# Kernel tuning notes

Measured on AMD Instinct MI355X. Metric: run time of the kernel, lower is better.

## Reference

```python
import jax, jax.numpy as jnp
from jax import lax
import numpy as np

B, T, D, U, K = 32, 1000, 512, 5, 3  # batch, frames, idim, upsample_times, conv kernel (l_order+r_order+1)
THRESHOLD = 1.0
TAIL = 0.45


def setup_inputs() -> dict:
    key = jax.random.key(0)
    ks = jax.random.split(key, 6)
    return {
        "encoder_out": jax.random.normal(ks[0], (B, T, D), jnp.float32),
        "mask": jnp.ones((B, 1, T), jnp.float32),
        "conv_w": jax.random.normal(ks[1], (D, D, K), jnp.float32) * 0.02,  # torch Conv1d [out,in,k]
        "conv_b": jnp.zeros((D,), jnp.float32),
        "up_w": jax.random.normal(ks[2], (D, D, U), jnp.float32) * 0.02,    # torch ConvTranspose1d [in,out,k]
        "up_b": jnp.zeros((D,), jnp.float32),
        "w1": jax.random.normal(ks[3], (D,), jnp.float32) * 0.05,           # cif_output Linear(D,1)
        "b1": jnp.zeros((), jnp.float32),
        "w2": jax.random.normal(ks[4], (D,), jnp.float32) * 0.05,           # cif_output2 Linear(D,1)
        "b2": jnp.zeros((), jnp.float32),
    }


def _cif(hidden, alphas, threshold):
    # hidden: [B, Tt, D], alphas: [B, Tt]
    Bb, Tt, Dd = hidden.shape

    def step(carry, inp):
        integrate, frame = carry
        alpha, h_t = inp  # [B], [B, D]
        dist_completion = 1.0 - integrate
        integrate = integrate + alpha
        fires_t = integrate
        fire = integrate >= threshold
        integrate = jnp.where(fire, integrate - 1.0, integrate)
        cur = jnp.where(fire, dist_completion, alpha)
        frame_out = frame + cur[:, None] * h_t
        frame = jnp.where(fire[:, None], (alpha - cur)[:, None] * h_t, frame_out)
        return (integrate, frame), (fires_t, frame_out)

    init = (jnp.zeros((Bb,), hidden.dtype), jnp.zeros((Bb, Dd), hidden.dtype))
    _, (fires, frames) = lax.scan(step, init, (alphas.T, jnp.swapaxes(hidden, 0, 1)))
    fires = fires.T                      # [B, Tt]
    frames = jnp.swapaxes(frames, 0, 1)  # [B, Tt, D]

    fire_mask = fires >= threshold

    def gather_b(frames_b, mask_b):
        pos = jnp.cumsum(mask_b.astype(jnp.int32)) - 1
        pos = jnp.where(mask_b, pos, Tt)  # non-fires -> out of range, dropped
        return jnp.zeros((Tt, Dd), frames_b.dtype).at[pos].set(frames_b, mode='drop')

    acoustic = jax.vmap(gather_b)(frames, fire_mask)  # [B, Tt, D] zero-padded
    return acoustic, fires


def reference(encoder_out, mask, conv_w, conv_b, up_w, up_b, w1, b1, w2, b2):
    Bb, Tt, Dd = encoder_out.shape
    context = jnp.swapaxes(encoder_out, 1, 2)           # [B, D, T]
    queries = jnp.pad(context, ((0, 0), (0, 0), (1, 1)))  # ConstantPad1d((1,1))
    conv = lax.conv_general_dilated(queries, conv_w, (1,), 'VALID',
                                    dimension_numbers=('NCH', 'OIH', 'NCH'))
    output = jax.nn.relu(conv + conv_b[None, :, None])  # [B, D, T]

    # ConvTranspose1d(stride=kernel=U, pad=0): non-overlapping -> einsum
    out2 = jnp.einsum('bit,ioj->btjo', output, up_w).reshape(Bb, Tt * U, Dd) + up_b  # [B, T*U, D]
    alphas2 = jax.nn.relu(jax.nn.sigmoid(out2 @ w2 + b2) * 1.0 - 0.0)  # smooth_factor2=1, noise_threshold2=0
    mask2 = jnp.swapaxes(jnp.broadcast_to(mask, (Bb, U, Tt)), 1, 2).reshape(Bb, Tt * U)
    alphas2 = alphas2 * mask2
    token_num2 = alphas2.sum(-1)

    h1 = jnp.swapaxes(output, 1, 2)  # [B, T, D]
    alphas = jax.nn.relu(jax.nn.sigmoid(h1 @ w1 + b1) * 1.0 - 0.0)  # smooth_factor=1, noise_threshold=0
    maskT = jnp.swapaxes(mask, 1, 2)[..., 0]  # [B, T]
    alphas = alphas * maskT

    # tail_process_fn (tail_threshold=0.45, mask given)
    zeros_t = jnp.zeros((Bb, 1), alphas.dtype)
    ones_t = jnp.ones((Bb, 1), alphas.dtype)
    mask_1 = jnp.concatenate([maskT, zeros_t], axis=1)
    mask_2 = jnp.concatenate([ones_t, maskT], axis=1)
    tail_add = (mask_2 - mask_1) * TAIL
    alphas_t = jnp.concatenate([alphas, zeros_t], axis=1) + tail_add  # [B, T+1]
    hidden = jnp.concatenate([encoder_out, jnp.zeros((Bb, 1, Dd), encoder_out.dtype)], axis=1)
    token_num = jnp.floor(alphas_t.sum(-1))

    acoustic_embeds, cif_peak = _cif(hidden, alphas_t, THRESHOLD)
    return acoustic_embeds, token_num, alphas_t, cif_peak, token_num2
```

## Files before the change

### kernel.cpp

```cpp
#include <hip/hip_runtime.h>
#include <math.h>

#define TB 32
#define TT 1000
#define TD 512
#define TU 5
#define TT1 1001

#define OFF_ACC  0
#define OFF_TOKN 16400384
#define OFF_ALPH 16400416
#define OFF_PEAK 16432448
#define OFF_TOK2 16464480

typedef _Float16 half8 __attribute__((ext_vector_type(8)));
typedef _Float16 half2t __attribute__((ext_vector_type(2)));
typedef float float4t __attribute__((ext_vector_type(4)));

typedef __attribute__((address_space(3))) uint32_t lds_u32_t;
typedef __attribute__((address_space(1))) const uint32_t g_u32_t;
#define GLOAD_LDS(gp, lp) __builtin_amdgcn_global_load_lds((g_u32_t*)(gp), (lds_u32_t*)(lp), 16, 0, 0)

#define BSTR 72
#define ASTR 200
#define EROWS 1032

#define WS_ARAW1 0
#define WS_ARAW2 32000
#define WS_VMAT  192000
#define WS_C2    194560
#define WS_WA    194564
#define WS_WB    226596
#define WS_FIRE  258628
#define WS_NF    290660
#define WS_ENCS_BYTES 1163264ull
#define WS_CWS_BYTES  (WS_ENCS_BYTES + 76059648ull)
#define WS_NEED_BYTES (WS_CWS_BYTES + 3276800ull)

__global__ __launch_bounds__(256) void kzero(float* araw1, float* araw2, float* tok2) {
    int idx = blockIdx.x * 256 + threadIdx.x;
    int stride = gridDim.x * 256;
    for (int i = idx; i < TB * TT; i += stride) araw1[i] = 0.f;
    for (int i = idx; i < TB * TT * TU; i += stride) araw2[i] = 0.f;
    if (idx < TB) tok2[idx] = 0.f;
}

__global__ __launch_bounds__(256) void kc2(const float* __restrict__ up_b, const float* __restrict__ w2,
                                           const float* __restrict__ b2, float* __restrict__ c2out) {
    int tid = threadIdx.x;
    float p = 0.f;
    for (int o = tid; o < TD; o += 256) p += up_b[o] * w2[o];
#pragma unroll
    for (int m = 1; m < 64; m <<= 1) p += __shfl_xor(p, m);
    __shared__ float wsum[4];
    if ((tid & 63) == 0) wsum[tid >> 6] = p;
    __syncthreads();
    if (tid == 0) c2out[0] = b2[0] + wsum[0] + wsum[1] + wsum[2] + wsum[3];
}

__global__ __launch_bounds__(64) void kv(const float* __restrict__ up_w, const float* __restrict__ w2,
                                         float* __restrict__ vmat) {
    int i = blockIdx.x, lane = threadIdx.x;
    float s0 = 0, s1 = 0, s2 = 0, s3 = 0, s4 = 0;
    for (int o = lane; o < TD; o += 64) {
        float w = w2[o];
        const float* p = up_w + (size_t)i * (TD * TU) + o * TU;
        s0 += p[0] * w; s1 += p[1] * w; s2 += p[2] * w; s3 += p[3] * w; s4 += p[4] * w;
    }
#pragma unroll
    for (int m = 1; m < 64; m <<= 1) {
        s0 += __shfl_xor(s0, m); s1 += __shfl_xor(s1, m); s2 += __shfl_xor(s2, m);
        s3 += __shfl_xor(s3, m); s4 += __shfl_xor(s4, m);
    }
    if (lane == 0) {
        float* d = vmat + i * TU;
        d[0] = s0; d[1] = s1; d[2] = s2; d[3] = s3; d[4] = s4;
    }
}

#define FILL_BLOCKS (256 + 1024)
__global__ __launch_bounds__(256) void kfill(float* araw1, float* araw2, float* tok2,
                                             _Float16* encs) {
    int bid = blockIdx.x, tid = threadIdx.x;
    if (bid < 256) {
        int idx = bid * 256 + tid;
        int stride = 256 * 256;
        for (int i = idx; i < TB * TT; i += stride) araw1[i] = 0.f;
        for (int i = idx; i < TB * TT * TU; i += stride) araw2[i] = 0.f;
        if (idx < TB) tok2[idx] = 0.f;
    } else {
        uint32_t* p = (uint32_t*)encs;
        int idx = (bid - 256) * 256 + tid;
        int stride = 1024 * 256;
        const int total = 512 * 32 * 36;
        for (int u = idx; u < total; u += stride) {
            int bic = u / (32 * 36);
            int r = (u / 36) % 32;
            int w = u % 36;
            int row = (r == 0) ? 0 : 1000 + r;
            p[((size_t)bic * EROWS + row) * 36 + w] = 0u;
        }
    }
}

#define WV_BLOCKS (TD + TD)
__global__ __launch_bounds__(64) void kwv(const float* __restrict__ up_w, const float* __restrict__ w2,
                                          const float* __restrict__ cw,
                                          float* __restrict__ vmat, _Float16* __restrict__ cws) {
    int bid = blockIdx.x, lane = threadIdx.x;
    if (bid < TD) {
        int i = bid;
        float s0 = 0, s1 = 0, s2 = 0, s3 = 0, s4 = 0;
        for (int o = lane; o < TD; o += 64) {
            float w = w2[o];
            const float* p = up_w + (size_t)i * (TD * TU) + o * TU;
            s0 += p[0] * w; s1 += p[1] * w; s2 += p[2] * w; s3 += p[3] * w; s4 += p[4] * w;
        }
#pragma unroll
        for (int m = 1; m < 64; m <<= 1) {
            s0 += __shfl_xor(s0, m); s1 += __shfl_xor(s1, m); s2 += __shfl_xor(s2, m);
            s3 += __shfl_xor(s3, m); s4 += __shfl_xor(s4, m);
        }
        if (lane == 0) {
            float* d = vmat + i * TU;
            d[0] = s0; d[1] = s1; d[2] = s2; d[3] = s3; d[4] = s4;
        }
    } else {
        int o = bid - TD;
        for (int u = lane; u < 16 * 32 * 3; u += 64) {
            int tap = u % 3, pos = (u / 3) % 32, ic = u / 96;
            float x = cw[((size_t)o * TD + ic * 32 + pos) * 3 + tap];
            _Float16 h = (_Float16)x;
            _Float16 l = (_Float16)(x - (float)h);
            size_t base = (((size_t)(o >> 5) * 16 + ic) * 32 + (o & 31)) * ASTR + tap * 64;
            cws[base + pos] = h;
            cws[base + 32 + pos] = l;
        }
    }
}

__global__ __launch_bounds__(256) void ksplitE(const float* __restrict__ enc, _Float16* __restrict__ encs) {
    int t = blockIdx.x, b = blockIdx.y, tid = threadIdx.x;
    int c = tid * 2;
    const float2 x2 = *(const float2*)&enc[((size_t)b * TT + t) * TD + c];
    float x0 = x2.x, x1 = x2.y;
    _Float16 h0 = (_Float16)x0, h1 = (_Float16)x1;
    _Float16 l0 = (_Float16)(x0 - (float)h0), l1 = (_Float16)(x1 - (float)h1);
    int ic = c >> 5, pos = c & 31;
    size_t base = ((size_t)(b * 16 + ic) * EROWS + 1 + t) * BSTR + pos;
    half2t hh; hh[0] = h0; hh[1] = h1;
    half2t ll; ll[0] = l0; ll[1] = l1;
    *(half2t*)&encs[base] = hh;
    *(half2t*)&encs[base + 32] = ll;
}

__global__ __launch_bounds__(256, 2) void kconvMD(const _Float16* __restrict__ encs,
                                                  const _Float16* __restrict__ cws,
                                                  const float* __restrict__ cb, const float* __restrict__ w1,
                                                  const float* __restrict__ vmat,
                                                  float* __restrict__ araw1, float* __restrict__ araw2) {
    __shared__ _Float16 sB[258 * BSTR];
    __shared__ _Float16 sA[64 * ASTR];

    const int tid = threadIdx.x;
    const int t0 = blockIdx.x * 256;
    const int oc = blockIdx.y;
    const int b = blockIdx.z;
    const int o0 = oc * 64;
    const int wv = tid >> 6, lane = tid & 63;
    const int q = lane >> 4, l15 = lane & 15;

    float4t acc[4][4];
#pragma unroll
    for (int i = 0; i < 4; ++i)
#pragma unroll
        for (int j = 0; j < 4; ++j) acc[i][j] = (float4t){0.f, 0.f, 0.f, 0.f};

    for (int ic = 0; ic < 16; ++ic) {
        __syncthreads();
        const _Float16* gB = encs + ((size_t)(b * 16 + ic) * EROWS + t0) * BSTR;
        for (int c = tid; c < 2322; c += 256) GLOAD_LDS(gB + c * 8, &sB[c * 8]);
        const _Float16* gA0 = cws + ((size_t)((oc * 2 + 0) * 16 + ic) * 32) * ASTR;
        const _Float16* gA1 = cws + ((size_t)((oc * 2 + 1) * 16 + ic) * 32) * ASTR;
        for (int c = tid; c < 800; c += 256) GLOAD_LDS(gA0 + c * 8, &sA[c * 8]);
        for (int c = tid; c < 800; c += 256) GLOAD_LDS(gA1 + c * 8, &sA[6400 + c * 8]);
        __syncthreads();
#pragma unroll
        for (int tap = 0; tap < 3; ++tap) {
            half8 Bh[4], Bl[4];
#pragma unroll
            for (int tt = 0; tt < 4; ++tt) {
                int s = wv * 64 + tt * 16 + l15 + tap;
                Bh[tt] = *(const half8*)&sB[s * BSTR + q * 8];
                Bl[tt] = *(const half8*)&sB[s * BSTR + 32 + q * 8];
            }
#pragma unroll
            for (int ot = 0; ot < 4; ++ot) {
                const int orow = ot * 16 + l15;
                half8 Ah = *(const half8*)&sA[orow * ASTR + tap * 64 + q * 8];
                half8 Al = *(const half8*)&sA[orow * ASTR + tap * 64 + 32 + q * 8];
#pragma unroll
                for (int tt = 0; tt < 4; ++tt) {
                    acc[ot][tt] = __builtin_amdgcn_mfma_f32_16x16x32_f16(Ah, Bh[tt], acc[ot][tt], 0, 0, 0);
                    acc[ot][tt] = __builtin_amdgcn_mfma_f32_16x16x32_f16(Ah, Bl[tt], acc[ot][tt], 0, 0, 0);
                    acc[ot][tt] = __builtin_amdgcn_mfma_f32_16x16x32_f16(Al, Bh[tt], acc[ot][tt], 0, 0, 0);
                }
            }
        }
    }

#pragma unroll
    for (int tt = 0; tt < 4; ++tt) {
        int t = t0 + wv * 64 + tt * 16 + l15;
        float s1 = 0.f, sa = 0.f, sb = 0.f, sc = 0.f, sd = 0.f, se = 0.f;
#pragma unroll
        for (int ot = 0; ot < 4; ++ot) {
#pragma unroll
            for (int r = 0; r < 4; ++r) {
                int o = o0 + ot * 16 + q * 4 + r;
                float rv = fmaxf(acc[ot][tt][r] + cb[o], 0.f);
                s1 = fmaf(w1[o], rv, s1);
                const float* vp = &vmat[o * 5];
                sa = fmaf(vp[0], rv, sa); sb = fmaf(vp[1], rv, sb);
                sc = fmaf(vp[2], rv, sc); sd = fmaf(vp[3], rv, sd);
                se = fmaf(vp[4], rv, se);
            }
        }
        s1 += __shfl_xor(s1, 16); sa += __shfl_xor(sa, 16); sb += __shfl_xor(sb, 16);
        sc += __shfl_xor(sc, 16); sd += __shfl_xor(sd, 16); se += __shfl_xor(se, 16);
        s1 += __shfl_xor(s1, 32); sa += __shfl_xor(sa, 32); sb += __shfl_xor(sb, 32);
        sc += __shfl_xor(sc, 32); sd += __shfl_xor(sd, 32); se += __shfl_xor(se, 32);
        if (q == 0 && t < TT) {
            atomicAdd(&araw1[b * TT + t], s1);
            float* p2 = &araw2[(b * TT + t) * 5];
            atomicAdd(p2 + 0, sa); atomicAdd(p2 + 1, sb); atomicAdd(p2 + 2, sc);
            atomicAdd(p2 + 3, sd); atomicAdd(p2 + 4, se);
        }
    }
}

__global__ __launch_bounds__(256, 3) void kconvM(const float* __restrict__ enc, const float* __restrict__ cw,
                                                 const float* __restrict__ cb, const float* __restrict__ w1,
                                                 const float* __restrict__ vmat,
                                                 float* __restrict__ araw1, float* __restrict__ araw2) {
    __shared__ _Float16 sB[258 * BSTR];
    __shared__ _Float16 sA[32 * ASTR];

    const int tid = threadIdx.x;
    const int t0 = blockIdx.x * 256;
    const int o0 = blockIdx.y * 32;
    const int b = blockIdx.z;
    const int wv = tid >> 6, lane = tid & 63;
    const int q = lane >> 4, l15 = lane & 15;

    float4t acc[2][4];
#pragma unroll
    for (int i = 0; i < 2; ++i)
#pragma unroll
        for (int j = 0; j < 4; ++j) acc[i][j] = (float4t){0.f, 0.f, 0.f, 0.f};

    for (int i0 = 0; i0 < TD; i0 += 32) {
        __syncthreads();
        for (int u = tid; u < 258 * 16; u += 256) {
            int s = u >> 4, ii2 = (u & 15) << 1;
            int t = t0 - 1 + s;
            float x0 = 0.f, x1 = 0.f;
            if (t >= 0 && t < TT) {
                const float* p = &enc[((size_t)b * TT + t) * TD + i0 + ii2];
                x0 = p[0]; x1 = p[1];
            }
            _Float16 h0 = (_Float16)x0, h1 = (_Float16)x1;
            _Float16 l0 = (_Float16)(x0 - (float)h0), l1 = (_Float16)(x1 - (float)h1);
            half2t hh; hh[0] = h0; hh[1] = h1;
            half2t ll; ll[0] = l0; ll[1] = l1;
            *(half2t*)&sB[s * BSTR + ii2] = hh;
            *(half2t*)&sB[s * BSTR + 32 + ii2] = ll;
        }
        for (int u = tid; u < 32 * 16; u += 256) {
            int o = u >> 4, ii2 = (u & 15) << 1;
            const float* p = &cw[((size_t)(o0 + o) * TD + i0 + ii2) * 3];
#pragma unroll
            for (int k = 0; k < 3; ++k) {
                float x0 = p[k], x1 = p[3 + k];
                _Float16 h0 = (_Float16)x0, h1 = (_Float16)x1;
                _Float16 l0 = (_Float16)(x0 - (float)h0), l1 = (_Float16)(x1 - (float)h1);
                half2t hh; hh[0] = h0; hh[1] = h1;
                half2t ll; ll[0] = l0; ll[1] = l1;
                *(half2t*)&sA[o * ASTR + k * 64 + ii2] = hh;
                *(half2t*)&sA[o * ASTR + k * 64 + 32 + ii2] = ll;
            }
        }
        __syncthreads();
#pragma unroll
        for (int tap = 0; tap < 3; ++tap) {
            half8 Bh[4], Bl[4];
#pragma unroll
            for (int tt = 0; tt < 4; ++tt) {
                int s = wv * 64 + tt * 16 + l15 + tap;
                Bh[tt] = *(const half8*)&sB[s * BSTR + q * 8];
                Bl[tt] = *(const half8*)&sB[s * BSTR + 32 + q * 8];
            }
#pragma unroll
            for (int ot = 0; ot < 2; ++ot) {
                const int orow = ot * 16 + l15;
                half8 Ah = *(const half8*)&sA[orow * ASTR + tap * 64 + q * 8];
                half8 Al = *(const half8*)&sA[orow * ASTR + tap * 64 + 32 + q * 8];
#pragma unroll
                for (int tt = 0; tt < 4; ++tt) {
                    acc[ot][tt] = __builtin_amdgcn_mfma_f32_16x16x32_f16(Ah, Bh[tt], acc[ot][tt], 0, 0, 0);
                    acc[ot][tt] = __builtin_amdgcn_mfma_f32_16x16x32_f16(Ah, Bl[tt], acc[ot][tt], 0, 0, 0);
                    acc[ot][tt] = __builtin_amdgcn_mfma_f32_16x16x32_f16(Al, Bh[tt], acc[ot][tt], 0, 0, 0);
                }
            }
        }
    }

#pragma unroll
    for (int tt = 0; tt < 4; ++tt) {
        int t = t0 + wv * 64 + tt * 16 + l15;
        float s1 = 0.f, sa = 0.f, sb = 0.f, sc = 0.f, sd = 0.f, se = 0.f;
#pragma unroll
        for (int ot = 0; ot < 2; ++ot) {
#pragma unroll
            for (int r = 0; r < 4; ++r) {
                int o = o0 + ot * 16 + q * 4 + r;
                float rv = fmaxf(acc[ot][tt][r] + cb[o], 0.f);
                s1 = fmaf(w1[o], rv, s1);
                const float* vp = &vmat[o * 5];
                sa = fmaf(vp[0], rv, sa); sb = fmaf(vp[1], rv, sb);
                sc = fmaf(vp[2], rv, sc); sd = fmaf(vp[3], rv, sd);
                se = fmaf(vp[4], rv, se);
            }
        }
        s1 += __shfl_xor(s1, 16); sa += __shfl_xor(sa, 16); sb += __shfl_xor(sb, 16);
        sc += __shfl_xor(sc, 16); sd += __shfl_xor(sd, 16); se += __shfl_xor(se, 16);
        s1 += __shfl_xor(s1, 32); sa += __shfl_xor(sa, 32); sb += __shfl_xor(sb, 32);
        sc += __shfl_xor(sc, 32); sd += __shfl_xor(sd, 32); se += __shfl_xor(se, 32);
        if (q == 0 && t < TT) {
            atomicAdd(&araw1[b * TT + t], s1);
            float* p2 = &araw2[(b * TT + t) * 5];
            atomicAdd(p2 + 0, sa); atomicAdd(p2 + 1, sb); atomicAdd(p2 + 2, sc);
            atomicAdd(p2 + 3, sd); atomicAdd(p2 + 4, se);
        }
    }
}

#define STEP(j, aj) { \
    float dist = 1.f - integ; \
    integ += (aj); \
    sp[tq + (j)] = integ; \
    bool fire = integ >= 1.f; \
    float cur = fire ? dist : (aj); \
    swa[tq + (j)] = cur; \
    swb[tq + (j)] = fire ? ((aj) - cur) : 0.f; \
    if (fire) { sf[F++] = tq + (j); integ -= 1.f; } \
    Ssum += (aj); }

__global__ __launch_bounds__(64) void kscan(const float* __restrict__ araw1, const float* __restrict__ araw2,
                                            const float* __restrict__ mask, const float* __restrict__ b1,
                                            const float* __restrict__ c2,
                                            float* __restrict__ alphas_t,
                                            float* __restrict__ cif_peak, float* __restrict__ token_num,
                                            float* __restrict__ tok2,
                                            float* __restrict__ wA, float* __restrict__ wB,
                                            int* __restrict__ fire_time, int* __restrict__ n_fires) {
    __shared__ float sa[TT1 + 7], sp[TT1], swa[TT1], swb[TT1];
    __shared__ int sf[TT1];
    __shared__ int sFs;
    int b = blockIdx.x, lane = threadIdx.x;

    const float cc = c2[0];
    const float b1v = b1[0];
    float sum5 = 0.f;
    for (int t = lane; t < TT1 + 7; t += 64) {
        float av = 0.f;
        if (t < TT) {
            float mk = mask[b * TT + t];
            float a1 = araw1[b * TT + t] + b1v;
            float alpha = mk / (1.f + expf(-a1));
            float mprev = (t == 0) ? 1.f : mask[b * TT + t - 1];
            float tail = (mprev - mk) * 0.45f;
            av = alpha + tail;
            float x0 = araw2[(b * TT + t) * 5 + 0] + cc;
            float x1 = araw2[(b * TT + t) * 5 + 1] + cc;
            float x2 = araw2[(b * TT + t) * 5 + 2] + cc;
            float x3 = araw2[(b * TT + t) * 5 + 3] + cc;
            float x4 = araw2[(b * TT + t) * 5 + 4] + cc;
            sum5 += mk / (1.f + expf(-x0)) + mk / (1.f + expf(-x1)) + mk / (1.f + expf(-x2))
                  + mk / (1.f + expf(-x3)) + mk / (1.f + expf(-x4));
        } else if (t == TT) {
            av = mask[b * TT + TT - 1] * 0.45f;
        }
        sa[t] = (t < TT1) ? av : 0.f;
        if (t < TT1) alphas_t[b * TT1 + t] = av;
    }
#pragma unroll
    for (int m = 1; m < 64; m <<= 1) sum5 += __shfl_xor(sum5, m);
    if (lane == 0) tok2[b] = sum5;
    __syncthreads();

    if (lane == 0) {
        float integ = 0.f, Ssum = 0.f;
        int F = 0;
        for (int tq = 0; tq < TT1 - 1; tq += 8) {
            float a0 = sa[tq], a1 = sa[tq + 1], a2 = sa[tq + 2], a3 = sa[tq + 3];
            float a4 = sa[tq + 4], a5 = sa[tq + 5], a6 = sa[tq + 6], a7 = sa[tq + 7];
            STEP(0, a0) STEP(1, a1) STEP(2, a2) STEP(3, a3)
            STEP(4, a4) STEP(5, a5) STEP(6, a6) STEP(7, a7)
        }
        { int tq = TT1 - 1; float a0 = sa[tq]; STEP(0, a0) }
        token_num[b] = floorf(Ssum);
        n_fires[b] = F;
        sFs = F;
    }
    __syncthreads();
    int F = sFs;
    for (int t = lane; t < TT1; t += 64) {
        cif_peak[b * TT1 + t] = sp[t];
        wA[b * TT1 + t] = swa[t];
        wB[b * TT1 + t] = swb[t];
        if (t < F) fire_time[b * TT1 + t] = sf[t];
    }
}

__global__ __launch_bounds__(128) void kgather(const float* __restrict__ enc,
                                               const float* __restrict__ wA, const float* __restrict__ wB,
                                               const int* __restrict__ fire_time, const int* __restrict__ n_fires,
                                               float* __restrict__ acoustic) {
    int k = blockIdx.x, b = blockIdx.y;
    int d4 = threadIdx.x;
    float ox = 0.f, oy = 0.f, oz = 0.f, ow = 0.f;
    int nf = n_fires[b];
    if (k < nf) {
        int end = fire_time[b * TT1 + k];
        int start = (k > 0) ? fire_time[b * TT1 + k - 1] : 0;
        for (int t = start; t <= end; ++t) {
            if (t >= TT) continue;
            float w = (k > 0 && t == start) ? wB[b * TT1 + t] : wA[b * TT1 + t];
            float4 h = ((const float4*)(enc + ((size_t)b * TT + t) * TD))[d4];
            ox += w * h.x; oy += w * h.y; oz += w * h.z; ow += w * h.w;
        }
    }
    float4 o4; o4.x = ox; o4.y = oy; o4.z = oz; o4.w = ow;
    ((float4*)(acoustic + ((size_t)b * TT1 + k) * TD))[d4] = o4;
}

extern "C" void kernel_launch(void* const* d_in, const int* in_sizes, int n_in,
                              void* d_out, int out_size, void* d_ws, size_t ws_size,
                              hipStream_t stream) {
    (void)in_sizes; (void)n_in; (void)out_size;
    const float* enc = (const float*)d_in[0];
    const float* mask = (const float*)d_in[1];
    const float* cw = (const float*)d_in[2];
    const float* cb = (const float*)d_in[3];
    const float* upw = (const float*)d_in[4];
    const float* upb = (const float*)d_in[5];
    const float* w1 = (const float*)d_in[6];
    const float* b1 = (const float*)d_in[7];
    const float* w2 = (const float*)d_in[8];
    const float* b2 = (const float*)d_in[9];

    float* out = (float*)d_out;
    float* acoustic = out + OFF_ACC;
    float* token_num = out + OFF_TOKN;
    float* alphas_t = out + OFF_ALPH;
    float* cif_peak = out + OFF_PEAK;
    float* tok2 = out + OFF_TOK2;

    float* ws = (float*)d_ws;
    float* araw1 = ws + WS_ARAW1;
    float* araw2 = ws + WS_ARAW2;
    float* vmat = ws + WS_VMAT;
    float* c2 = ws + WS_C2;
    float* wA = ws + WS_WA;
    float* wB = ws + WS_WB;
    int* fire_time = (int*)(ws + WS_FIRE);
    int* n_fires = (int*)(ws + WS_NF);
    _Float16* encs = (_Float16*)((char*)d_ws + WS_ENCS_BYTES);
    _Float16* cws = (_Float16*)((char*)d_ws + WS_CWS_BYTES);

    const bool bigws = (ws_size >= WS_NEED_BYTES);

    if (bigws) {
        hipLaunchKernelGGL(kfill, dim3(FILL_BLOCKS), dim3(256), 0, stream, araw1, araw2, tok2, encs);
        hipLaunchKernelGGL(ksplitE, dim3(TT, TB), dim3(256), 0, stream, enc, encs);
        hipLaunchKernelGGL(kc2, dim3(1), dim3(256), 0, stream, upb, w2, b2, c2);
        hipLaunchKernelGGL(kwv, dim3(WV_BLOCKS), dim3(64), 0, stream, upw, w2, cw, vmat, cws);
        hipLaunchKernelGGL(kconvMD, dim3(4, 8, TB), dim3(256), 0, stream, encs, cws, cb, w1, vmat, araw1, araw2);
    } else {
        hipLaunchKernelGGL(kzero, dim3(256), dim3(256), 0, stream, araw1, araw2, tok2);
        hipLaunchKernelGGL(kc2, dim3(1), dim3(256), 0, stream, upb, w2, b2, c2);
        hipLaunchKernelGGL(kv, dim3(TD), dim3(64), 0, stream, upw, w2, vmat);
        hipLaunchKernelGGL(kconvM, dim3(4, 16, TB), dim3(256), 0, stream, enc, cw, cb, w1, vmat, araw1, araw2);
    }
    hipLaunchKernelGGL(kscan, dim3(TB), dim3(64), 0, stream, araw1, araw2, mask, b1, c2,
                       alphas_t, cif_peak, token_num, tok2, wA, wB, fire_time, n_fires);
    hipLaunchKernelGGL(kgather, dim3(TT1, TB), dim3(128), 0, stream, enc, wA, wB, fire_time, n_fires, acoustic);
}
```

Baseline: 385.9 us.

## Enlarge conv MFMA block tile to 256 output channels with 512 threads

The fused conv kernel now computes 256 output channels per block instead of 64, using 512 threads arranged as 4 time-groups by 2 output-halves. Each wave accumulates 8x4 MFMA tiles. The encoder slab loaded into LDS is therefore reused across four times as many output channels, which cuts global and LDS traffic for the B operand, and the grid shrinks to 256 blocks. The cost is roughly 140 KB of dynamic LDS per block and 128 accumulator registers per lane. Under launch bounds of (512, 2) that register demand may force spills, and at most one block can fit per CU.

```diff
diff --git a/kernel.cpp b/kernel.cpp
--- a/kernel.cpp
+++ b/kernel.cpp
@@ -24,6 +24,9 @@
 #define BSTR 72
 #define ASTR 200
 #define EROWS 1032
+
+#define SB_HALVES 18576
+#define SMEM_BYTES ((SB_HALVES + 256 * ASTR) * 2)
 
 #define WS_ARAW1 0
 #define WS_ARAW2 32000
@@ -154,70 +157,78 @@
     *(half2t*)&encs[base + 32] = ll;
 }
 
-__global__ __launch_bounds__(256, 2) void kconvMD(const _Float16* __restrict__ encs,
+__global__ __launch_bounds__(512, 2) void kconvMD(const _Float16* __restrict__ encs,
                                                   const _Float16* __restrict__ cws,
                                                   const float* __restrict__ cb, const float* __restrict__ w1,
                                                   const float* __restrict__ vmat,
                                                   float* __restrict__ araw1, float* __restrict__ araw2) {
-    __shared__ _Float16 sB[258 * BSTR];
-    __shared__ _Float16 sA[64 * ASTR];
+    extern __shared__ _Float16 smem[];
+    _Float16* sB = smem;
+    _Float16* sA = smem + SB_HALVES;
 
     const int tid = threadIdx.x;
     const int t0 = blockIdx.x * 256;
-    const int oc = blockIdx.y;
+    const int oc8 = blockIdx.y * 8;
     const int b = blockIdx.z;
-    const int o0 = oc * 64;
+    const int o0 = blockIdx.y * 256;
     const int wv = tid >> 6, lane = tid & 63;
+    const int wt = wv & 3;
+    const int wo = wv >> 2;
     const int q = lane >> 4, l15 = lane & 15;
 
-    float4t acc[4][4];
-#pragma unroll
-    for (int i = 0; i < 4; ++i)
+    float4t acc[8][4];
+#pragma unroll
+    for (int i = 0; i < 8; ++i)
 #pragma unroll
         for (int j = 0; j < 4; ++j) acc[i][j] = (float4t){0.f, 0.f, 0.f, 0.f};
 
+#pragma unroll 1
     for (int ic = 0; ic < 16; ++ic) {
         __syncthreads();
         const _Float16* gB = encs + ((size_t)(b * 16 + ic) * EROWS + t0) * BSTR;
-        for (int c = tid; c < 2322; c += 256) GLOAD_LDS(gB + c * 8, &sB[c * 8]);
-        const _Float16* gA0 = cws + ((size_t)((oc * 2 + 0) * 16 + ic) * 32) * ASTR;
-        const _Float16* gA1 = cws + ((size_t)((oc * 2 + 1) * 16 + ic) * 32) * ASTR;
-        for (int c = tid; c < 800; c += 256) GLOAD_LDS(gA0 + c * 8, &sA[c * 8]);
-        for (int c = tid; c < 800; c += 256) GLOAD_LDS(gA1 + c * 8, &sA[6400 + c * 8]);
+        for (int c = tid; c < 2322; c += 512) GLOAD_LDS(gB + c * 8, &sB[c * 8]);
+#pragma unroll
+        for (int g = 0; g < 8; ++g) {
+            const _Float16* gA = cws + ((size_t)((oc8 + g) * 16 + ic) * 32) * ASTR;
+            for (int c = tid; c < 800; c += 512) GLOAD_LDS(gA + c * 8, &sA[g * 6400 + c * 8]);
+        }
         __syncthreads();
 #pragma unroll
         for (int tap = 0; tap < 3; ++tap) {
             half8 Bh[4], Bl[4];
 #pragma unroll
             for (int tt = 0; tt < 4; ++tt) {
-                int s = wv * 64 + tt * 16 + l15 + tap;
+                int s = wt * 64 + tt * 16 + l15 + tap;
                 Bh[tt] = *(const half8*)&sB[s * BSTR + q * 8];
                 Bl[tt] = *(const half8*)&sB[s * BSTR + 32 + q * 8];
             }
 #pragma unroll
-            for (int ot = 0; ot < 4; ++ot) {
-                const int orow = ot * 16 + l15;
+            for (int ot = 0; ot < 8; ++ot) {
+                const int orow = wo * 128 + ot * 16 + l15;
                 half8 Ah = *(const half8*)&sA[orow * ASTR + tap * 64 + q * 8];
                 half8 Al = *(const half8*)&sA[orow * ASTR + tap * 64 + 32 + q * 8];
 #pragma unroll
-                for (int tt = 0; tt < 4; ++tt) {
+                for (int tt = 0; tt < 4; ++tt)
                     acc[ot][tt] = __builtin_amdgcn_mfma_f32_16x16x32_f16(Ah, Bh[tt], acc[ot][tt], 0, 0, 0);
+#pragma unroll
+                for (int tt = 0; tt < 4; ++tt)
                     acc[ot][tt] = __builtin_amdgcn_mfma_f32_16x16x32_f16(Ah, Bl[tt], acc[ot][tt], 0, 0, 0);
+#pragma unroll
+                for (int tt = 0; tt < 4; ++tt)
                     acc[ot][tt] = __builtin_amdgcn_mfma_f32_16x16x32_f16(Al, Bh[tt], acc[ot][tt], 0, 0, 0);
-                }
             }
         }
     }
 
 #pragma unroll
     for (int tt = 0; tt < 4; ++tt) {
-        int t = t0 + wv * 64 + tt * 16 + l15;
+        int t = t0 + wt * 64 + tt * 16 + l15;
         float s1 = 0.f, sa = 0.f, sb = 0.f, sc = 0.f, sd = 0.f, se = 0.f;
 #pragma unroll
-        for (int ot = 0; ot < 4; ++ot) {
+        for (int ot = 0; ot < 8; ++ot) {
 #pragma unroll
             for (int r = 0; r < 4; ++r) {
-                int o = o0 + ot * 16 + q * 4 + r;
+                int o = o0 + wo * 128 + ot * 16 + q * 4 + r;
                 float rv = fmaxf(acc[ot][tt][r] + cb[o], 0.f);
                 s1 = fmaf(w1[o], rv, s1);
                 const float* vp = &vmat[o * 5];
@@ -481,12 +492,20 @@
 
     const bool bigws = (ws_size >= WS_NEED_BYTES);
 
+    static bool attr_set = false;
+    if (!attr_set) {
+        hipFuncSetAttribute(reinterpret_cast<const void*>(&kconvMD),
+                            hipFuncAttributeMaxDynamicSharedMemorySize, SMEM_BYTES);
+        attr_set = true;
+    }
+
     if (bigws) {
         hipLaunchKernelGGL(kfill, dim3(FILL_BLOCKS), dim3(256), 0, stream, araw1, araw2, tok2, encs);
         hipLaunchKernelGGL(ksplitE, dim3(TT, TB), dim3(256), 0, stream, enc, encs);
         hipLaunchKernelGGL(kc2, dim3(1), dim3(256), 0, stream, upb, w2, b2, c2);
         hipLaunchKernelGGL(kwv, dim3(WV_BLOCKS), dim3(64), 0, stream, upw, w2, cw, vmat, cws);
-        hipLaunchKernelGGL(kconvMD, dim3(4, 8, TB), dim3(256), 0, stream, encs, cws, cb, w1, vmat, araw1, araw2);
+        hipLaunchKernelGGL(kconvMD, dim3(4, 2, TB), dim3(512), SMEM_BYTES, stream,
+                           encs, cws, cb, w1, vmat, araw1, araw2);
     } else {
         hipLaunchKernelGGL(kzero, dim3(256), dim3(256), 0, stream, araw1, araw2, tok2);
         hipLaunchKernelGGL(kc2, dim3(1), dim3(256), 0, stream, upb, w2, b2, c2);
```

Result: no change. 390.6 us (+1.2%).
